# Kernel optimization log

Hardware: AMD Instinct MI355X
Metric: run time of the kernel (lower is better)

The kernel has to match this reference:

```python
import jax, jax.numpy as jnp
import numpy as np

NU, NI, D, B, L, E = 100000, 50000, 128, 3, 2, 1500000
N = NU + NI  # total nodes
EPS = 1e-5


def setup_inputs() -> dict:
    key = jax.random.key(0)
    ks = jax.random.split(key, 20)
    s = 0.05  # xavier-ish scale for 128-dim layers
    inp = {}
    inp["edge_index"] = jax.random.randint(ks[0], (2, E), 0, N, dtype=jnp.int32)
    inp["edge_type"] = jax.random.randint(ks[1], (E,), 0, B, dtype=jnp.int32)
    inp["item_feats"] = jax.random.normal(ks[2], (NI, D), jnp.float32)
    inp["user_emb"] = jax.random.normal(ks[3], (NU, D), jnp.float32) * s
    inp["user_proj_W"] = jax.random.normal(ks[4], (D, D), jnp.float32) * s
    inp["user_proj_b"] = jnp.zeros((D,), jnp.float32)
    inp["item_proj_W"] = jax.random.normal(ks[5], (D, D), jnp.float32) * s
    inp["item_proj_b"] = jnp.zeros((D,), jnp.float32)
    # stacked SAGEConv params: lin_l (neighbor, with bias) and lin_r (root, no bias)
    inp["sage_Wl"] = jax.random.normal(ks[6], (B, L, D, D), jnp.float32) * s
    inp["sage_bl"] = jnp.zeros((B, L, D), jnp.float32)
    inp["sage_Wr"] = jax.random.normal(ks[7], (B, L, D, D), jnp.float32) * s
    inp["bn_gamma"] = jnp.ones((B, L, D), jnp.float32)
    inp["bn_beta"] = jnp.zeros((B, L, D), jnp.float32)
    inp["query_W"] = jax.random.normal(ks[8], (D, D), jnp.float32) * s
    inp["query_b"] = jnp.zeros((D,), jnp.float32)
    inp["key_W"] = jax.random.normal(ks[9], (B, D, D), jnp.float32) * s
    inp["key_b"] = jnp.zeros((B, D), jnp.float32)
    inp["fuse_W"] = jax.random.normal(ks[10], (D, D), jnp.float32) * s
    inp["fuse_b"] = jnp.zeros((D,), jnp.float32)
    inp["refine_W"] = jax.random.normal(ks[11], (D, D), jnp.float32) * s
    inp["refine_b"] = jnp.zeros((D,), jnp.float32)
    return inp


def reference(edge_index, edge_type, item_feats, user_emb,
              user_proj_W, user_proj_b, item_proj_W, item_proj_b,
              sage_Wl, sage_bl, sage_Wr, bn_gamma, bn_beta,
              query_W, query_b, key_W, key_b,
              fuse_W, fuse_b, refine_W, refine_b):
    # initial node features: projected user embeddings + projected item feats
    x = jnp.concatenate([user_emb @ user_proj_W + user_proj_b,
                         item_feats @ item_proj_W + item_proj_b], axis=0)  # [N, D]
    src, dst = edge_index[0], edge_index[1]
    outs = []
    for b in range(B):
        # redirect edges of other behaviours to a dummy segment N (dropped)
        dst_b = jnp.where(edge_type == b, dst, N)
        cnt = jax.ops.segment_sum(jnp.ones((E,), x.dtype), dst_b, num_segments=N + 1)[:N]
        denom = jnp.maximum(cnt, 1.0)[:, None]
        h = x
        for l in range(L):
            # SAGEConv: mean-aggregate neighbor messages + root transform
            agg = jax.ops.segment_sum(h[src], dst_b, num_segments=N + 1)[:N] / denom
            h = agg @ sage_Wl[b, l] + sage_bl[b, l] + h @ sage_Wr[b, l]
            # BatchNorm1d (training-mode batch statistics, biased variance)
            mu = h.mean(axis=0)
            var = h.var(axis=0)
            h = (h - mu) * jax.lax.rsqrt(var + EPS) * bn_gamma[b, l] + bn_beta[b, l]
            if l < L - 1:
                h = jax.nn.relu(h)
        outs.append(x + h)  # residual
    stack = jnp.stack(outs, axis=0)  # [B, N, D]
    # attention fusion across behaviours
    Q = x @ query_W + query_b                                   # [N, D]
    K = jnp.einsum('bnd,bde->bne', stack, key_W) + key_b[:, None, :]  # [B, N, D]
    logits = jnp.einsum('nd,bnd->nb', Q, K)                      # [N, B]
    w = jax.nn.softmax(logits, axis=-1)
    fused = jnp.einsum('nb,bnd->nd', w, stack)
    fused = fused @ fuse_W + fuse_b
    # refine: Linear + ReLU (dropout is identity in eval)
    return jax.nn.relu(fused @ refine_W + refine_b)
```

## Files before the change

### kernel.cpp

```cpp
#include <hip/hip_runtime.h>

#define NUSER 100000
#define NITEM 50000
#define NNODE 150000
#define DIM 128
#define NB 3
#define NL 2
#define BN_EPS 1e-5f
#define NT3P 450560
#define SCAN_BLOCKS 440
#define TILESN 2344
#define NT32 4688
#define BNABLK 9375

typedef unsigned short u16;
typedef _Float16 f16;
typedef __attribute__((ext_vector_type(8))) _Float16 f16x8;
typedef __attribute__((ext_vector_type(8))) unsigned short us8;
typedef __attribute__((ext_vector_type(4))) float f32x4;

__device__ __forceinline__ float h2f(u16 u) { f16 h; __builtin_memcpy(&h, &u, 2); return (float)h; }
__device__ __forceinline__ u16 f2h(float f) { f16 h = (f16)f; u16 u; __builtin_memcpy(&u, &h, 2); return u; }

struct Out3 { u16* p[3]; };
struct WPtrs { const float* s[8]; };


__global__ __launch_bounds__(256) void count_edges(const int* __restrict__ ei,
                                                   const int* __restrict__ et, int E,
                                                   int* __restrict__ cnt) {
    int t = blockIdx.x * 256 + threadIdx.x;
    if (t >= E) return;
    atomicAdd(&cnt[et[t] * NNODE + ei[E + t]], 1);
}

__global__ __launch_bounds__(256) void scan1(const int* __restrict__ cnt, int* __restrict__ bsum) {
    __shared__ int sh[256];
    int tid = threadIdx.x;
    int base = blockIdx.x * 1024 + tid * 4;
    int4 v = *(const int4*)(cnt + base);
    sh[tid] = v.x + v.y + v.z + v.w;
    __syncthreads();
    for (int off = 128; off > 0; off >>= 1) {
        if (tid < off) sh[tid] += sh[tid + off];
        __syncthreads();
    }
    if (tid == 0) bsum[blockIdx.x] = sh[0];
}

__global__ __launch_bounds__(512) void scan2(int* __restrict__ bsum, int nb) {
    __shared__ int sh[512];
    int tid = threadIdx.x;
    sh[tid] = (tid < nb) ? bsum[tid] : 0;
    __syncthreads();
    for (int off = 1; off < 512; off <<= 1) {
        int v = sh[tid];
        int add = (tid >= off) ? sh[tid - off] : 0;
        __syncthreads();
        sh[tid] = v + add;
        __syncthreads();
    }
    if (tid < nb) bsum[tid] = (tid == 0) ? 0 : sh[tid - 1];
}

__global__ __launch_bounds__(256) void scan3(const int* __restrict__ cnt, const int* __restrict__ bsum,
                                             int* __restrict__ row_start, int* __restrict__ cur) {
    __shared__ int sh[256];
    int tid = threadIdx.x;
    int base = blockIdx.x * 1024 + tid * 4;
    int4 v = *(const int4*)(cnt + base);
    sh[tid] = v.x + v.y + v.z + v.w;
    __syncthreads();
    for (int off = 1; off < 256; off <<= 1) {
        int a = sh[tid];
        int add = (tid >= off) ? sh[tid - off] : 0;
        __syncthreads();
        sh[tid] = a + add;
        __syncthreads();
    }
    int excl = ((tid == 0) ? 0 : sh[tid - 1]) + bsum[blockIdx.x];
    int4 o;
    o.x = excl; o.y = excl + v.x; o.z = o.y + v.y; o.w = o.z + v.z;
    *(int4*)(row_start + base) = o;
    *(int4*)(cur + base) = o;
}

__global__ __launch_bounds__(256) void scatter_csr(const int* __restrict__ ei,
                                                   const int* __restrict__ et, int E,
                                                   int* __restrict__ cur, int* __restrict__ adj) {
    int t = blockIdx.x * 256 + threadIdx.x;
    if (t >= E) return;
    int pos = atomicAdd(&cur[et[t] * NNODE + ei[E + t]], 1);
    adj[pos] = ei[t];
}


__global__ __launch_bounds__(256) void wconv_all(WPtrs w, u16* __restrict__ dst) {
    int gid = blockIdx.x * 256 + threadIdx.x;
    if (gid >= 20 * 16384) return;
    int m = gid >> 14, idx = gid & 16383;
    int k = idx & 127, n = idx >> 7;
    const float* src; int li;
    if (m == 0)       { src = w.s[0]; li = 0; }
    else if (m == 1)  { src = w.s[1]; li = 0; }
    else if (m < 8)   { src = w.s[2]; li = m - 2; }
    else if (m < 14)  { src = w.s[3]; li = m - 8; }
    else if (m == 14) { src = w.s[4]; li = 0; }
    else if (m < 18)  { src = w.s[5]; li = m - 15; }
    else if (m == 18) { src = w.s[6]; li = 0; }
    else              { src = w.s[7]; li = 0; }
    dst[(size_t)m * 16384 + idx] = f2h(src[(size_t)li * 16384 + k * 128 + n]);
}


__global__ __launch_bounds__(256) void bn_apply(u16* __restrict__ h,
                                                const float* __restrict__ stats6,
                                                const float* __restrict__ gamma,
                                                const float* __restrict__ beta) {
    __shared__ float sc[DIM];
    __shared__ float sf[DIM];
    const int tid = threadIdx.x;
    const int b = blockIdx.x / BNABLK;
    const int blk = blockIdx.x % BNABLK;
    const int bl = b * NL;
    if (tid < DIM) {
        const float* st = stats6 + bl * 256;
        const float invN = 1.0f / (float)NNODE;
        float mu = st[tid] * invN;
        float var = fmaxf(st[DIM + tid] * invN - mu * mu, 0.f);
        float scv = gamma[bl * DIM + tid] * rsqrtf(var + BN_EPS);
        sc[tid] = scv;
        sf[tid] = beta[bl * DIM + tid] - mu * scv;
    }
    __syncthreads();
    const int i = blk * 256 + tid;
    const int c8 = (i & 15) * 8;
    u16* p = h + (size_t)b * NNODE * DIM + (size_t)i * 8;
    us8 u = *(const us8*)p;
    us8 o;
#pragma unroll
    for (int j = 0; j < 8; ++j)
        o[j] = f2h(fmaxf(h2f(u[j]) * sc[c8 + j] + sf[c8 + j], 0.f));
    *(us8*)p = o;
}


__global__ __launch_bounds__(256, 6) void sage_layer(
    const u16* __restrict__ hin0, const u16* __restrict__ wt_Wl,
    const u16* __restrict__ wt_Wr, const float* __restrict__ sage_bl,
    float* __restrict__ stats6, Out3 outs, int layer,
    const int* __restrict__ adj, const int* __restrict__ row_start,
    const int* __restrict__ cnt) {
    __shared__ u16 T1[64][136];
    __shared__ float sstat[256];
    const int tid = threadIdx.x;
    const int b = blockIdx.x / TILESN;
    const int tile = blockIdx.x % TILESN;
    const int r0 = tile * 64;
    const int bl = b * NL + layer;
    const u16* hin = hin0 + (layer ? (size_t)b * NNODE * DIM : 0);
    const u16* Wl = wt_Wl + (size_t)bl * 16384;
    const u16* Wr = wt_Wr + (size_t)bl * 16384;

    sstat[tid] = 0.f;

    {
        const int lrow = tid >> 3;
        const int c0 = (tid & 7) * 16;
        for (int half = 0; half < 2; ++half) {
            const int row = lrow + half * 32;
            float a[16];
#pragma unroll
            for (int j = 0; j < 16; ++j) a[j] = 0.f;
            const int n = r0 + row;
            if (n < NNODE) {
                const int base = b * NNODE + n;
                const int s0 = row_start[base];
                const int deg = cnt[base];
                int e = 0;
                for (; e + 1 < deg; e += 2) {
                    const u16* p1 = hin + (size_t)adj[s0 + e] * DIM + c0;
                    const u16* p2 = hin + (size_t)adj[s0 + e + 1] * DIM + c0;
                    us8 u0 = *(const us8*)p1, u1 = *(const us8*)(p1 + 8);
                    us8 v0 = *(const us8*)p2, v1 = *(const us8*)(p2 + 8);
#pragma unroll
                    for (int j = 0; j < 8; ++j) {
                        a[j]     += h2f(u0[j]) + h2f(v0[j]);
                        a[8 + j] += h2f(u1[j]) + h2f(v1[j]);
                    }
                }
                if (e < deg) {
                    const u16* p1 = hin + (size_t)adj[s0 + e] * DIM + c0;
                    us8 u0 = *(const us8*)p1, u1 = *(const us8*)(p1 + 8);
#pragma unroll
                    for (int j = 0; j < 8; ++j) {
                        a[j]     += h2f(u0[j]);
                        a[8 + j] += h2f(u1[j]);
                    }
                }
                const float s = 1.0f / (float)(deg > 1 ? deg : 1);
#pragma unroll
                for (int j = 0; j < 16; ++j) a[j] *= s;
            }
            us8 o0, o1;
#pragma unroll
            for (int j = 0; j < 8; ++j) { o0[j] = f2h(a[j]); o1[j] = f2h(a[8 + j]); }
            *(us8*)&T1[row][c0] = o0;
            *(us8*)&T1[row][c0 + 8] = o1;
        }
    }
    __syncthreads();

    const int wave = tid >> 6, lane = tid & 63, q = lane >> 4, rlo = lane & 15;
    const f16x8 zf = (f16x8)(f16)0.f;
    f32x4 acc[4][2];
#pragma unroll
    for (int t = 0; t < 4; ++t) { acc[t][0] = (f32x4)0.f; acc[t][1] = (f32x4)0.f; }
#pragma unroll
    for (int kc = 0; kc < DIM; kc += 32) {
        f16x8 b1v[2], b2v[2];
#pragma unroll
        for (int c = 0; c < 2; ++c) {
            b1v[c] = *(const f16x8*)(Wl + (size_t)(wave * 32 + 16 * c + rlo) * DIM + kc + q * 8);
            b2v[c] = *(const f16x8*)(Wr + (size_t)(wave * 32 + 16 * c + rlo) * DIM + kc + q * 8);
        }
#pragma unroll
        for (int t = 0; t < 4; ++t) {
            f16x8 a1 = *(const f16x8*)&T1[16 * t + rlo][kc + q * 8];
            int rr = r0 + 16 * t + rlo;
            f16x8 a2 = (rr < NNODE) ? *(const f16x8*)(hin + (size_t)rr * DIM + kc + q * 8) : zf;
            acc[t][0] = __builtin_amdgcn_mfma_f32_16x16x32_f16(a1, b1v[0], acc[t][0], 0, 0, 0);
            acc[t][1] = __builtin_amdgcn_mfma_f32_16x16x32_f16(a1, b1v[1], acc[t][1], 0, 0, 0);
            acc[t][0] = __builtin_amdgcn_mfma_f32_16x16x32_f16(a2, b2v[0], acc[t][0], 0, 0, 0);
            acc[t][1] = __builtin_amdgcn_mfma_f32_16x16x32_f16(a2, b2v[1], acc[t][1], 0, 0, 0);
        }
    }

    const int col0 = wave * 32 + rlo, col1 = col0 + 16;
    const float bb0 = sage_bl[bl * DIM + col0], bb1 = sage_bl[bl * DIM + col1];
    const bool tiled = (layer == 1) && (b > 0);
    float rs0 = 0, rq0 = 0, rs1 = 0, rq1 = 0;
#pragma unroll
    for (int t = 0; t < 4; ++t) {
#pragma unroll
        for (int r = 0; r < 4; ++r) {
            int rloc = 16 * t + q * 4 + r;
            int row = r0 + rloc;
            if (row >= NNODE) continue;
            float v0 = acc[t][0][r] + bb0;
            float v1 = acc[t][1][r] + bb1;
            rs0 += v0; rq0 += v0 * v0; rs1 += v1; rq1 += v1 * v1;
            if (!tiled) {
                u16* C = outs.p[b];
                C[(size_t)row * DIM + col0] = f2h(v0);
                C[(size_t)row * DIM + col1] = f2h(v1);
            } else {
                int tt = row >> 5, rl = row & 31;
                u16* base = (tt == NT32 - 1) ? outs.p[2]
                                             : outs.p[1] + (size_t)tt * 8192;
                base += (size_t)(b - 1) * 4096 + rl * DIM;
                base[col0] = f2h(v0);
                base[col1] = f2h(v1);
            }
        }
    }
    rs0 += __shfl_xor(rs0, 16); rs0 += __shfl_xor(rs0, 32);
    rq0 += __shfl_xor(rq0, 16); rq0 += __shfl_xor(rq0, 32);
    rs1 += __shfl_xor(rs1, 16); rs1 += __shfl_xor(rs1, 32);
    rq1 += __shfl_xor(rq1, 16); rq1 += __shfl_xor(rq1, 32);
    if (q == 0) {
        atomicAdd(&sstat[col0], rs0);
        atomicAdd(&sstat[DIM + col0], rq0);
        atomicAdd(&sstat[col1], rs1);
        atomicAdd(&sstat[DIM + col1], rq1);
    }
    __syncthreads();
    if (tid < DIM) {
        float* so = stats6 + bl * 256;
        atomicAdd(&so[tid], sstat[tid]);
        atomicAdd(&so[DIM + tid], sstat[DIM + tid]);
    }
}


__global__ __launch_bounds__(256) void attn_fuse(
    const u16* __restrict__ hpre0, const u16* __restrict__ hpre12,
    const u16* __restrict__ tailb, const float* __restrict__ stats6,
    const float* __restrict__ gamma, const float* __restrict__ beta,
    const u16* __restrict__ xh, const u16* __restrict__ wt,
    const float* __restrict__ query_b, const float* __restrict__ key_b,
    const float* __restrict__ fuse_b, const float* __restrict__ refine_b,
    float* __restrict__ out) {
    __shared__ __attribute__((aligned(16))) u16 St[3][32][136];
    __shared__ float sc[3][DIM], sf[3][DIM];
    __shared__ float slog[32][4];
    __shared__ float swt[32][4];
    const int tid = threadIdx.x;
    const int tile = blockIdx.x;
    const int r0 = tile * 32;
    const u16* wt_q    = wt + 14 * 16384;
    const u16* wt_key  = wt + 15 * 16384;
    const u16* wt_fuse = wt + 18 * 16384;
    const u16* wt_ref  = wt + 19 * 16384;

    if (tid < DIM) {
        const float invN = 1.0f / (float)NNODE;
#pragma unroll
        for (int b = 0; b < NB; ++b) {
            const int bl = b * NL + 1;
            const float* st = stats6 + bl * 256;
            float mu = st[tid] * invN;
            float var = fmaxf(st[DIM + tid] * invN - mu * mu, 0.f);
            float c = gamma[bl * DIM + tid] * rsqrtf(var + BN_EPS);
            sc[b][tid] = c;
            sf[b][tid] = beta[bl * DIM + tid] - mu * c;
        }
    }
    if (tid < 32) { slog[tid][0] = 0.f; slog[tid][1] = 0.f; slog[tid][2] = 0.f; }
    __syncthreads();

    for (int i = tid; i < 512; i += 256) {
        int r = i >> 4, c8 = (i & 15) * 8;
        int n = r0 + r;
        if (n < NNODE) {
            us8 xv = *(const us8*)(xh + (size_t)n * DIM + c8);
#pragma unroll
            for (int b = 0; b < NB; ++b) {
                const u16* src = (b == 0)
                    ? hpre0 + (size_t)n * DIM + c8
                    : ((tile == NT32 - 1) ? tailb : hpre12 + (size_t)tile * 8192)
                      + (size_t)(b - 1) * 4096 + r * DIM + c8;
                us8 hv = *(const us8*)src;
                us8 o;
#pragma unroll
                for (int j = 0; j < 8; ++j)
                    o[j] = f2h(h2f(hv[j]) * sc[b][c8 + j] + sf[b][c8 + j] + h2f(xv[j]));
                *(us8*)&St[b][r][c8] = o;
            }
        } else {
            us8 z = (us8)(u16)0;
#pragma unroll
            for (int b = 0; b < NB; ++b) *(us8*)&St[b][r][c8] = z;
        }
    }
    __syncthreads();

    const int wave = tid >> 6, lane = tid & 63, q = lane >> 4, rlo = lane & 15;
    const int col0 = wave * 32 + rlo, col1 = col0 + 16;
    const f16x8 zf = (f16x8)(f16)0.f;

    f32x4 qa[2][2];
#pragma unroll
    for (int t = 0; t < 2; ++t) { qa[t][0] = (f32x4)0.f; qa[t][1] = (f32x4)0.f; }
#pragma unroll
    for (int kc = 0; kc < DIM; kc += 32) {
        f16x8 bv0 = *(const f16x8*)(wt_q + (size_t)(wave * 32 + rlo) * DIM + kc + q * 8);
        f16x8 bv1 = *(const f16x8*)(wt_q + (size_t)(wave * 32 + 16 + rlo) * DIM + kc + q * 8);
#pragma unroll
        for (int t = 0; t < 2; ++t) {
            int rr = r0 + 16 * t + rlo;
            f16x8 av = (rr < NNODE) ? *(const f16x8*)(xh + (size_t)rr * DIM + kc + q * 8) : zf;
            qa[t][0] = __builtin_amdgcn_mfma_f32_16x16x32_f16(av, bv0, qa[t][0], 0, 0, 0);
            qa[t][1] = __builtin_amdgcn_mfma_f32_16x16x32_f16(av, bv1, qa[t][1], 0, 0, 0);
        }
    }
    {
        const float qb0 = query_b[col0], qb1 = query_b[col1];
#pragma unroll
        for (int t = 0; t < 2; ++t)
#pragma unroll
            for (int r = 0; r < 4; ++r) { qa[t][0][r] += qb0; qa[t][1][r] += qb1; }
    }

#pragma unroll
    for (int b = 0; b < NB; ++b) {
        f32x4 ka[2][2];
#pragma unroll
        for (int t = 0; t < 2; ++t) { ka[t][0] = (f32x4)0.f; ka[t][1] = (f32x4)0.f; }
        const u16* Wk = wt_key + (size_t)b * 16384;
#pragma unroll
        for (int kc = 0; kc < DIM; kc += 32) {
            f16x8 bv0 = *(const f16x8*)(Wk + (size_t)(wave * 32 + rlo) * DIM + kc + q * 8);
            f16x8 bv1 = *(const f16x8*)(Wk + (size_t)(wave * 32 + 16 + rlo) * DIM + kc + q * 8);
#pragma unroll
            for (int t = 0; t < 2; ++t) {
                f16x8 av = *(const f16x8*)&St[b][16 * t + rlo][kc + q * 8];
                ka[t][0] = __builtin_amdgcn_mfma_f32_16x16x32_f16(av, bv0, ka[t][0], 0, 0, 0);
                ka[t][1] = __builtin_amdgcn_mfma_f32_16x16x32_f16(av, bv1, ka[t][1], 0, 0, 0);
            }
        }
        const float kb0 = key_b[b * DIM + col0], kb1 = key_b[b * DIM + col1];
#pragma unroll
        for (int t = 0; t < 2; ++t) {
#pragma unroll
            for (int r = 0; r < 4; ++r) {
                int rloc = 16 * t + q * 4 + r;
                float v = (ka[t][0][r] + kb0) * qa[t][0][r]
                        + (ka[t][1][r] + kb1) * qa[t][1][r];
                v += __shfl_xor(v, 1);
                v += __shfl_xor(v, 2);
                v += __shfl_xor(v, 4);
                v += __shfl_xor(v, 8);
                if (rlo == 0) atomicAdd(&slog[rloc][b], v);
            }
        }
    }
    __syncthreads();

    if (tid < 32) {
        float l0 = slog[tid][0], l1 = slog[tid][1], l2 = slog[tid][2];
        float mm = fmaxf(l0, fmaxf(l1, l2));
        float e0 = expf(l0 - mm), e1 = expf(l1 - mm), e2 = expf(l2 - mm);
        float inv = 1.0f / (e0 + e1 + e2);
        swt[tid][0] = e0 * inv; swt[tid][1] = e1 * inv; swt[tid][2] = e2 * inv;
    }
    __syncthreads();

    f32x4 facc[2][2];
#pragma unroll
    for (int t = 0; t < 2; ++t) { facc[t][0] = (f32x4)0.f; facc[t][1] = (f32x4)0.f; }
#pragma unroll
    for (int b = 0; b < NB; ++b) {
        f32x4 ga[2][2];
#pragma unroll
        for (int t = 0; t < 2; ++t) { ga[t][0] = (f32x4)0.f; ga[t][1] = (f32x4)0.f; }
#pragma unroll
        for (int kc = 0; kc < DIM; kc += 32) {
            f16x8 bv0 = *(const f16x8*)(wt_fuse + (size_t)(wave * 32 + rlo) * DIM + kc + q * 8);
            f16x8 bv1 = *(const f16x8*)(wt_fuse + (size_t)(wave * 32 + 16 + rlo) * DIM + kc + q * 8);
#pragma unroll
            for (int t = 0; t < 2; ++t) {
                f16x8 av = *(const f16x8*)&St[b][16 * t + rlo][kc + q * 8];
                ga[t][0] = __builtin_amdgcn_mfma_f32_16x16x32_f16(av, bv0, ga[t][0], 0, 0, 0);
                ga[t][1] = __builtin_amdgcn_mfma_f32_16x16x32_f16(av, bv1, ga[t][1], 0, 0, 0);
            }
        }
#pragma unroll
        for (int t = 0; t < 2; ++t) {
#pragma unroll
            for (int r = 0; r < 4; ++r) {
                int rloc = 16 * t + q * 4 + r;
                float wgt = swt[rloc][b];
                facc[t][0][r] += wgt * ga[t][0][r];
                facc[t][1][r] += wgt * ga[t][1][r];
            }
        }
    }
    __syncthreads();

    {
        const float fb0 = fuse_b[col0], fb1 = fuse_b[col1];
#pragma unroll
        for (int t = 0; t < 2; ++t) {
#pragma unroll
            for (int r = 0; r < 4; ++r) {
                int rloc = 16 * t + q * 4 + r;
                St[0][rloc][col0] = f2h(facc[t][0][r] + fb0);
                St[0][rloc][col1] = f2h(facc[t][1][r] + fb1);
            }
        }
    }
    __syncthreads();

    f32x4 racc[2][2];
#pragma unroll
    for (int t = 0; t < 2; ++t) { racc[t][0] = (f32x4)0.f; racc[t][1] = (f32x4)0.f; }
#pragma unroll
    for (int kc = 0; kc < DIM; kc += 32) {
        f16x8 bv0 = *(const f16x8*)(wt_ref + (size_t)(wave * 32 + rlo) * DIM + kc + q * 8);
        f16x8 bv1 = *(const f16x8*)(wt_ref + (size_t)(wave * 32 + 16 + rlo) * DIM + kc + q * 8);
#pragma unroll
        for (int t = 0; t < 2; ++t) {
            f16x8 av = *(const f16x8*)&St[0][16 * t + rlo][kc + q * 8];
            racc[t][0] = __builtin_amdgcn_mfma_f32_16x16x32_f16(av, bv0, racc[t][0], 0, 0, 0);
            racc[t][1] = __builtin_amdgcn_mfma_f32_16x16x32_f16(av, bv1, racc[t][1], 0, 0, 0);
        }
    }
    {
        const float rb0 = refine_b[col0], rb1 = refine_b[col1];
#pragma unroll
        for (int t = 0; t < 2; ++t) {
#pragma unroll
            for (int r = 0; r < 4; ++r) {
                int row = r0 + 16 * t + q * 4 + r;
                if (row >= NNODE) continue;
                out[(size_t)row * DIM + col0] = fmaxf(racc[t][0][r] + rb0, 0.f);
                out[(size_t)row * DIM + col1] = fmaxf(racc[t][1][r] + rb1, 0.f);
            }
        }
    }
}


__global__ __launch_bounds__(256) void gemm_p(
    const void* __restrict__ Av, const u16* __restrict__ Wt,
    const float* __restrict__ bias, void* __restrict__ Cv, int M, int flags) {
    const u16* A16 = (const u16*)Av;
    const float* A32 = (const float*)Av;
    const float* bs = bias;
    const int r0 = blockIdx.x * 64;
    const int tid = threadIdx.x;
    const int wave = tid >> 6, lane = tid & 63, q = lane >> 4, rlo = lane & 15;
    f32x4 acc[4][2];
#pragma unroll
    for (int t = 0; t < 4; ++t) { acc[t][0] = (f32x4)0.f; acc[t][1] = (f32x4)0.f; }
    const f16x8 zf = (f16x8)(f16)0.f;
#pragma unroll
    for (int kc = 0; kc < DIM; kc += 32) {
        f16x8 av[4], bv[2];
#pragma unroll
        for (int t = 0; t < 4; ++t) {
            int row = r0 + 16 * t + rlo;
            if (row < M) {
                if (flags & 8) {
                    const float* p = A32 + (size_t)row * DIM + kc + q * 8;
                    float4 x0 = *(const float4*)p;
                    float4 x1 = *(const float4*)(p + 4);
                    f16x8 tmp;
                    tmp[0] = (f16)x0.x; tmp[1] = (f16)x0.y; tmp[2] = (f16)x0.z; tmp[3] = (f16)x0.w;
                    tmp[4] = (f16)x1.x; tmp[5] = (f16)x1.y; tmp[6] = (f16)x1.z; tmp[7] = (f16)x1.w;
                    av[t] = tmp;
                } else {
                    av[t] = *(const f16x8*)(A16 + (size_t)row * DIM + kc + q * 8);
                }
            } else {
                av[t] = zf;
            }
        }
#pragma unroll
        for (int c = 0; c < 2; ++c)
            bv[c] = *(const f16x8*)(Wt + (size_t)(wave * 32 + 16 * c + rlo) * DIM + kc + q * 8);
#pragma unroll
        for (int t = 0; t < 4; ++t) {
            acc[t][0] = __builtin_amdgcn_mfma_f32_16x16x32_f16(av[t], bv[0], acc[t][0], 0, 0, 0);
            acc[t][1] = __builtin_amdgcn_mfma_f32_16x16x32_f16(av[t], bv[1], acc[t][1], 0, 0, 0);
        }
    }

    const int col0 = wave * 32 + rlo, col1 = col0 + 16;
    const float bb0 = bs[col0], bb1 = bs[col1];
#pragma unroll
    for (int t = 0; t < 4; ++t) {
#pragma unroll
        for (int r = 0; r < 4; ++r) {
            int row = r0 + 16 * t + q * 4 + r;
            if (row >= M) continue;
            float v0 = acc[t][0][r] + bb0;
            float v1 = acc[t][1][r] + bb1;
            if (flags & 1) { v0 = fmaxf(v0, 0.f); v1 = fmaxf(v1, 0.f); }
            if (flags & 32) {
                ((u16*)Cv)[(size_t)row * DIM + col0] = f2h(v0);
                ((u16*)Cv)[(size_t)row * DIM + col1] = f2h(v1);
            } else {
                ((float*)Cv)[(size_t)row * DIM + col0] = v0;
                ((float*)Cv)[(size_t)row * DIM + col1] = v1;
            }
        }
    }
}


extern "C" void kernel_launch(void* const* d_in, const int* in_sizes, int n_in,
                              void* d_out, int out_size, void* d_ws, size_t ws_size,
                              hipStream_t stream) {
    const int* edge_index    = (const int*)d_in[0];
    const int* edge_type     = (const int*)d_in[1];
    const float* item_feats  = (const float*)d_in[2];
    const float* user_emb    = (const float*)d_in[3];
    const float* user_proj_b = (const float*)d_in[5];
    const float* item_proj_b = (const float*)d_in[7];
    const float* sage_bl  = (const float*)d_in[9];
    const float* bn_gamma = (const float*)d_in[11];
    const float* bn_beta  = (const float*)d_in[12];
    const float* query_b  = (const float*)d_in[14];
    const float* key_b    = (const float*)d_in[16];
    const float* fuse_b   = (const float*)d_in[18];
    const float* refine_b = (const float*)d_in[20];
    const int E = in_sizes[1];

    const size_t ND = (size_t)NNODE * DIM;
    char* w = (char*)d_ws;
    u16* xh = (u16*)w;          w += ND * 2;
    u16* stackb = (u16*)w;      w += NB * ND * 2;
    u16* fbuf = (u16*)w;        w += ND * 2;
    int* cnt = (int*)w;         w += (size_t)NT3P * 4;
    int* row_start = (int*)w;   w += (size_t)NT3P * 4;
    int* cur = (int*)w;         w += (size_t)NT3P * 4;
    int* adj = (int*)w;         w += (size_t)E * 4;
    u16* wt = (u16*)w;          w += (size_t)20 * 16384 * 2;
    int* bsum = (int*)w;        w += 2048;
    float* stats6 = (float*)w;  w += 6 * 256 * 4;
    u16* tailb = (u16*)w;       w += 16384;

    const u16* wt_user = wt;
    const u16* wt_item = wt + 16384;
    const u16* wt_Wl   = wt + 2 * 16384;
    const u16* wt_Wr   = wt + 8 * 16384;

    u16* dout16 = (u16*)d_out;

    hipMemsetAsync(cnt, 0, (size_t)NT3P * 4, stream);
    hipMemsetAsync(stats6, 0, 6 * 256 * 4, stream);
    int gE = (E + 255) / 256;
    count_edges<<<gE, 256, 0, stream>>>(edge_index, edge_type, E, cnt);
    scan1<<<SCAN_BLOCKS, 256, 0, stream>>>(cnt, bsum);
    scan2<<<1, 512, 0, stream>>>(bsum, SCAN_BLOCKS);
    scan3<<<SCAN_BLOCKS, 256, 0, stream>>>(cnt, bsum, row_start, cur);
    scatter_csr<<<gE, 256, 0, stream>>>(edge_index, edge_type, E, cur, adj);

    WPtrs wp;
    wp.s[0] = (const float*)d_in[4];
    wp.s[1] = (const float*)d_in[6];
    wp.s[2] = (const float*)d_in[8];
    wp.s[3] = (const float*)d_in[10];
    wp.s[4] = (const float*)d_in[13];
    wp.s[5] = (const float*)d_in[15];
    wp.s[6] = (const float*)d_in[17];
    wp.s[7] = (const float*)d_in[19];
    wconv_all<<<1280, 256, 0, stream>>>(wp, wt);

    const int TU = (NUSER + 63) / 64, TI = (NITEM + 63) / 64;
    gemm_p<<<TU, 256, 0, stream>>>(user_emb, wt_user, user_proj_b, xh, NUSER, 8 | 32);
    gemm_p<<<TI, 256, 0, stream>>>(item_feats, wt_item, item_proj_b,
                                   xh + (size_t)NUSER * DIM, NITEM, 8 | 32);

    Out3 out_l0, out_l1;
    for (int b = 0; b < NB; ++b) out_l0.p[b] = stackb + (size_t)b * ND;
    out_l1.p[0] = fbuf;
    out_l1.p[1] = dout16;
    out_l1.p[2] = tailb;

    sage_layer<<<NB * TILESN, 256, 0, stream>>>(xh, wt_Wl, wt_Wr, sage_bl,
                                                stats6, out_l0, 0,
                                                adj, row_start, cnt);
    bn_apply<<<NB * BNABLK, 256, 0, stream>>>(stackb, stats6, bn_gamma, bn_beta);
    sage_layer<<<NB * TILESN, 256, 0, stream>>>(stackb, wt_Wl, wt_Wr, sage_bl,
                                                stats6, out_l1, 1,
                                                adj, row_start, cnt);

    attn_fuse<<<NT32, 256, 0, stream>>>(fbuf, dout16, tailb, stats6,
                                        bn_gamma, bn_beta, xh, wt,
                                        query_b, key_b, fuse_b, refine_b,
                                        (float*)d_out);
}
```

Measured before the change: 1.018 ms.

## Fuse layer-0 BatchNorm+ReLU into layer-1 SAGE gather and root loads

Measured after the change: 1.180 ms. 15.9% more time.

```diff
diff --git a/kernel.cpp b/kernel.cpp
--- a/kernel.cpp
+++ b/kernel.cpp
@@ -11,7 +11,6 @@
 #define SCAN_BLOCKS 440
 #define TILESN 2344
 #define NT32 4688
-#define BNABLK 9375
 
 typedef unsigned short u16;
 typedef _Float16 f16;
@@ -24,6 +23,7 @@
 
 struct Out3 { u16* p[3]; };
 struct WPtrs { const float* s[8]; };
+template <bool B> struct BNC { static constexpr bool value = B; };
 
 
 __global__ __launch_bounds__(256) void count_edges(const int* __restrict__ ei,
@@ -113,45 +113,15 @@
 }
 
 
-__global__ __launch_bounds__(256) void bn_apply(u16* __restrict__ h,
-                                                const float* __restrict__ stats6,
-                                                const float* __restrict__ gamma,
-                                                const float* __restrict__ beta) {
-    __shared__ float sc[DIM];
-    __shared__ float sf[DIM];
-    const int tid = threadIdx.x;
-    const int b = blockIdx.x / BNABLK;
-    const int blk = blockIdx.x % BNABLK;
-    const int bl = b * NL;
-    if (tid < DIM) {
-        const float* st = stats6 + bl * 256;
-        const float invN = 1.0f / (float)NNODE;
-        float mu = st[tid] * invN;
-        float var = fmaxf(st[DIM + tid] * invN - mu * mu, 0.f);
-        float scv = gamma[bl * DIM + tid] * rsqrtf(var + BN_EPS);
-        sc[tid] = scv;
-        sf[tid] = beta[bl * DIM + tid] - mu * scv;
-    }
-    __syncthreads();
-    const int i = blk * 256 + tid;
-    const int c8 = (i & 15) * 8;
-    u16* p = h + (size_t)b * NNODE * DIM + (size_t)i * 8;
-    us8 u = *(const us8*)p;
-    us8 o;
-#pragma unroll
-    for (int j = 0; j < 8; ++j)
-        o[j] = f2h(fmaxf(h2f(u[j]) * sc[c8 + j] + sf[c8 + j], 0.f));
-    *(us8*)p = o;
-}
-
-
-__global__ __launch_bounds__(256, 6) void sage_layer(
+__global__ __launch_bounds__(256, 4) void sage_layer(
     const u16* __restrict__ hin0, const u16* __restrict__ wt_Wl,
     const u16* __restrict__ wt_Wr, const float* __restrict__ sage_bl,
+    const float* __restrict__ gamma, const float* __restrict__ beta,
     float* __restrict__ stats6, Out3 outs, int layer,
     const int* __restrict__ adj, const int* __restrict__ row_start,
     const int* __restrict__ cnt) {
     __shared__ u16 T1[64][136];
+    __shared__ float scb[DIM], sfb[DIM];
     __shared__ float sstat[256];
     const int tid = threadIdx.x;
     const int b = blockIdx.x / TILESN;
@@ -162,52 +132,93 @@
     const u16* Wl = wt_Wl + (size_t)bl * 16384;
     const u16* Wr = wt_Wr + (size_t)bl * 16384;
 
+    if (tid < DIM) {
+        float scv = 1.f, sfv = 0.f;
+        if (layer) {
+            const int bl0 = b * NL;
+            const float* st = stats6 + bl0 * 256;
+            const float invN = 1.0f / (float)NNODE;
+            float mu = st[tid] * invN;
+            float var = fmaxf(st[DIM + tid] * invN - mu * mu, 0.f);
+            scv = gamma[bl0 * DIM + tid] * rsqrtf(var + BN_EPS);
+            sfv = beta[bl0 * DIM + tid] - mu * scv;
+        }
+        scb[tid] = scv; sfb[tid] = sfv;
+    }
     sstat[tid] = 0.f;
+    __syncthreads();
 
     {
         const int lrow = tid >> 3;
         const int c0 = (tid & 7) * 16;
-        for (int half = 0; half < 2; ++half) {
-            const int row = lrow + half * 32;
-            float a[16];
-#pragma unroll
-            for (int j = 0; j < 16; ++j) a[j] = 0.f;
-            const int n = r0 + row;
-            if (n < NNODE) {
-                const int base = b * NNODE + n;
-                const int s0 = row_start[base];
-                const int deg = cnt[base];
-                int e = 0;
-                for (; e + 1 < deg; e += 2) {
-                    const u16* p1 = hin + (size_t)adj[s0 + e] * DIM + c0;
-                    const u16* p2 = hin + (size_t)adj[s0 + e + 1] * DIM + c0;
-                    us8 u0 = *(const us8*)p1, u1 = *(const us8*)(p1 + 8);
-                    us8 v0 = *(const us8*)p2, v1 = *(const us8*)(p2 + 8);
-#pragma unroll
-                    for (int j = 0; j < 8; ++j) {
-                        a[j]     += h2f(u0[j]) + h2f(v0[j]);
-                        a[8 + j] += h2f(u1[j]) + h2f(v1[j]);
+        auto run = [&](auto bnc) {
+            constexpr bool BN = decltype(bnc)::value;
+            float scl[16], shf[16];
+            if constexpr (BN) {
+#pragma unroll
+                for (int j = 0; j < 16; ++j) { scl[j] = scb[c0 + j]; shf[j] = sfb[c0 + j]; }
+            }
+            for (int half = 0; half < 2; ++half) {
+                const int row = lrow + half * 32;
+                float a[16];
+#pragma unroll
+                for (int j = 0; j < 16; ++j) a[j] = 0.f;
+                const int n = r0 + row;
+                if (n < NNODE) {
+                    const int base = b * NNODE + n;
+                    const int s0 = row_start[base];
+                    const int deg = cnt[base];
+                    auto accU = [&](us8 u0, us8 u1) {
+#pragma unroll
+                        for (int j = 0; j < 8; ++j) {
+                            float y0 = h2f(u0[j]), y1 = h2f(u1[j]);
+                            if constexpr (BN) {
+                                y0 = fmaxf(y0 * scl[j] + shf[j], 0.f);
+                                y1 = fmaxf(y1 * scl[8 + j] + shf[8 + j], 0.f);
+                            }
+                            a[j] += y0; a[8 + j] += y1;
+                        }
+                    };
+                    int e = 0;
+                    for (; e + 3 < deg; e += 4) {
+                        const int i0 = adj[s0 + e],     i1 = adj[s0 + e + 1];
+                        const int i2 = adj[s0 + e + 2], i3 = adj[s0 + e + 3];
+                        const u16* p0 = hin + (size_t)i0 * DIM + c0;
+                        const u16* p1 = hin + (size_t)i1 * DIM + c0;
+                        const u16* p2 = hin + (size_t)i2 * DIM + c0;
+                        const u16* p3 = hin + (size_t)i3 * DIM + c0;
+                        us8 u00 = *(const us8*)p0, u01 = *(const us8*)(p0 + 8);
+                        us8 u10 = *(const us8*)p1, u11 = *(const us8*)(p1 + 8);
+                        us8 u20 = *(const us8*)p2, u21 = *(const us8*)(p2 + 8);
+                        us8 u30 = *(const us8*)p3, u31 = *(const us8*)(p3 + 8);
+                        accU(u00, u01); accU(u10, u11); accU(u20, u21); accU(u30, u31);
                     }
+                    if (e + 1 < deg) {
+                        const u16* p0 = hin + (size_t)adj[s0 + e] * DIM + c0;
+                        const u16* p1 = hin + (size_t)adj[s0 + e + 1] * DIM + c0;
+                        us8 u00 = *(const us8*)p0, u01 = *(const us8*)(p0 + 8);
+                        us8 u10 = *(const us8*)p1, u11 = *(const us8*)(p1 + 8);
+                        accU(u00, u01); accU(u10, u11);
+                        e += 2;
+                    }
+                    if (e < deg) {
+                        const u16* p0 = hin + (size_t)adj[s0 + e] * DIM + c0;
+                        us8 u00 = *(const us8*)p0, u01 = *(const us8*)(p0 + 8);
+                        accU(u00, u01);
+                    }
+                    const float s = 1.0f / (float)(deg > 1 ? deg : 1);
+#pragma unroll
+                    for (int j = 0; j < 16; ++j) a[j] *= s;
                 }
-                if (e < deg) {
-                    const u16* p1 = hin + (size_t)adj[s0 + e] * DIM + c0;
-                    us8 u0 = *(const us8*)p1, u1 = *(const us8*)(p1 + 8);
-#pragma unroll
-                    for (int j = 0; j < 8; ++j) {
-                        a[j]     += h2f(u0[j]);
-                        a[8 + j] += h2f(u1[j]);
-                    }
-                }
-                const float s = 1.0f / (float)(deg > 1 ? deg : 1);
-#pragma unroll
-                for (int j = 0; j < 16; ++j) a[j] *= s;
-            }
-            us8 o0, o1;
-#pragma unroll
-            for (int j = 0; j < 8; ++j) { o0[j] = f2h(a[j]); o1[j] = f2h(a[8 + j]); }
-            *(us8*)&T1[row][c0] = o0;
-            *(us8*)&T1[row][c0 + 8] = o1;
-        }
+                us8 o0, o1;
+#pragma unroll
+                for (int j = 0; j < 8; ++j) { o0[j] = f2h(a[j]); o1[j] = f2h(a[8 + j]); }
+                *(us8*)&T1[row][c0] = o0;
+                *(us8*)&T1[row][c0 + 8] = o1;
+            }
+        };
+        if (layer) run(BNC<true>{});
+        else       run(BNC<false>{});
     }
     __syncthreads();
 
@@ -224,11 +235,33 @@
             b1v[c] = *(const f16x8*)(Wl + (size_t)(wave * 32 + 16 * c + rlo) * DIM + kc + q * 8);
             b2v[c] = *(const f16x8*)(Wr + (size_t)(wave * 32 + 16 * c + rlo) * DIM + kc + q * 8);
         }
+        float scA[8], sfA[8];
+        if (layer) {
+#pragma unroll
+            for (int j = 0; j < 8; ++j) {
+                scA[j] = scb[kc + q * 8 + j];
+                sfA[j] = sfb[kc + q * 8 + j];
+            }
+        }
 #pragma unroll
         for (int t = 0; t < 4; ++t) {
             f16x8 a1 = *(const f16x8*)&T1[16 * t + rlo][kc + q * 8];
             int rr = r0 + 16 * t + rlo;
-            f16x8 a2 = (rr < NNODE) ? *(const f16x8*)(hin + (size_t)rr * DIM + kc + q * 8) : zf;
+            f16x8 a2;
+            if (rr < NNODE) {
+                us8 u = *(const us8*)(hin + (size_t)rr * DIM + kc + q * 8);
+                if (layer) {
+                    f16x8 tmp;
+#pragma unroll
+                    for (int j = 0; j < 8; ++j)
+                        tmp[j] = (f16)fmaxf(h2f(u[j]) * scA[j] + sfA[j], 0.f);
+                    a2 = tmp;
+                } else {
+                    __builtin_memcpy(&a2, &u, 16);
+                }
+            } else {
+                a2 = zf;
+            }
             acc[t][0] = __builtin_amdgcn_mfma_f32_16x16x32_f16(a1, b1v[0], acc[t][0], 0, 0, 0);
             acc[t][1] = __builtin_amdgcn_mfma_f32_16x16x32_f16(a1, b1v[1], acc[t][1], 0, 0, 0);
             acc[t][0] = __builtin_amdgcn_mfma_f32_16x16x32_f16(a2, b2v[0], acc[t][0], 0, 0, 0);
@@ -330,7 +363,7 @@
                     ? hpre0 + (size_t)n * DIM + c8
                     : ((tile == NT32 - 1) ? tailb : hpre12 + (size_t)tile * 8192)
                       + (size_t)(b - 1) * 4096 + r * DIM + c8;
-                us8 hv = *(const us8*)src;
+                us8 hv = __builtin_nontemporal_load((const us8*)src);
                 us8 o;
 #pragma unroll
                 for (int j = 0; j < 8; ++j)
@@ -484,8 +517,10 @@
             for (int r = 0; r < 4; ++r) {
                 int row = r0 + 16 * t + q * 4 + r;
                 if (row >= NNODE) continue;
-                out[(size_t)row * DIM + col0] = fmaxf(racc[t][0][r] + rb0, 0.f);
-                out[(size_t)row * DIM + col1] = fmaxf(racc[t][1][r] + rb1, 0.f);
+                __builtin_nontemporal_store(fmaxf(racc[t][0][r] + rb0, 0.f),
+                                            &out[(size_t)row * DIM + col0]);
+                __builtin_nontemporal_store(fmaxf(racc[t][1][r] + rb1, 0.f),
+                                            &out[(size_t)row * DIM + col1]);
             }
         }
     }
@@ -514,11 +549,11 @@
             if (row < M) {
                 if (flags & 8) {
                     const float* p = A32 + (size_t)row * DIM + kc + q * 8;
-                    float4 x0 = *(const float4*)p;
-                    float4 x1 = *(const float4*)(p + 4);
+                    f32x4 x0 = __builtin_nontemporal_load((const f32x4*)p);
+                    f32x4 x1 = __builtin_nontemporal_load((const f32x4*)(p + 4));
                     f16x8 tmp;
-                    tmp[0] = (f16)x0.x; tmp[1] = (f16)x0.y; tmp[2] = (f16)x0.z; tmp[3] = (f16)x0.w;
-                    tmp[4] = (f16)x1.x; tmp[5] = (f16)x1.y; tmp[6] = (f16)x1.z; tmp[7] = (f16)x1.w;
+                    tmp[0] = (f16)x0[0]; tmp[1] = (f16)x0[1]; tmp[2] = (f16)x0[2]; tmp[3] = (f16)x0[3];
+                    tmp[4] = (f16)x1[0]; tmp[5] = (f16)x1[1]; tmp[6] = (f16)x1[2]; tmp[7] = (f16)x1[3];
                     av[t] = tmp;
                 } else {
                     av[t] = *(const f16x8*)(A16 + (size_t)row * DIM + kc + q * 8);
@@ -631,10 +666,11 @@
     out_l1.p[2] = tailb;
 
     sage_layer<<<NB * TILESN, 256, 0, stream>>>(xh, wt_Wl, wt_Wr, sage_bl,
+                                                bn_gamma, bn_beta,
                                                 stats6, out_l0, 0,
                                                 adj, row_start, cnt);
-    bn_apply<<<NB * BNABLK, 256, 0, stream>>>(stackb, stats6, bn_gamma, bn_beta);
     sage_layer<<<NB * TILESN, 256, 0, stream>>>(stackb, wt_Wl, wt_Wr, sage_bl,
+                                                bn_gamma, bn_beta,
                                                 stats6, out_l1, 1,
                                                 adj, row_start, cnt);
 
```
